# Kernel tuning notes

Hardware: AMD Instinct MI355X
Metric: run time of the kernel (lower is better)

The kernel has to match this reference:

```python
import jax, jax.numpy as jnp
import numpy as np

N = 8000   # nodes
E = 32000  # edges
B = 64     # graphs in batch
V = 5000   # vocab
D = 200    # embed dim; 20 tokens/node * 200 = 4000 = conv1 in_dim
T = 20


def setup_inputs() -> dict:
    key = jax.random.key(0)
    ks = jax.random.split(key, 12)
    return {
        "x": jax.random.randint(ks[0], (N, T), 0, V),
        "edge_index": jax.random.randint(ks[1], (2, E), 0, N),
        "batch": jnp.sort(jax.random.randint(ks[2], (N,), 0, B)),
        "emb": jax.random.normal(ks[3], (V, D), jnp.float32) * 0.02,
        "W1": jax.random.normal(ks[4], (4000, 6000), jnp.float32) * 0.01,
        "b1": jnp.zeros((6000,), jnp.float32),
        "W2": jax.random.normal(ks[5], (6000, 6000), jnp.float32) * 0.01,
        "b2": jnp.zeros((6000,), jnp.float32),
        "Wl1": jax.random.normal(ks[6], (6000, 3000), jnp.float32) * 0.01,
        "bl1": jnp.zeros((3000,), jnp.float32),
        "Wl2": jax.random.normal(ks[7], (3000, 4), jnp.float32) * 0.01,
        "bl2": jnp.zeros((4,), jnp.float32),
    }


def gcn_conv(h, W, b, src, dst, n):
    """PyG GCNConv: x' = D^-1/2 (A+I) D^-1/2 (x W) + b; src/dst include self-loops."""
    h = h @ W  # [n, out]
    deg = jax.ops.segment_sum(jnp.ones(dst.shape[0], h.dtype), dst, num_segments=n)
    dinv = jnp.where(deg > 0, jax.lax.rsqrt(deg), 0.0)
    norm = dinv[src] * dinv[dst]  # [E+n]
    agg = jax.ops.segment_sum(h[src] * norm[:, None], dst, num_segments=n)
    return agg + b


def reference(x, edge_index, batch, emb, W1, b1, W2, b2, Wl1, bl1, Wl2, bl2):
    n = x.shape[0]
    h = emb[x].reshape(n, -1)  # [N, 4000]
    loops = jnp.arange(n)
    src = jnp.concatenate([edge_index[0], loops])
    dst = jnp.concatenate([edge_index[1], loops])
    h = jax.nn.leaky_relu(gcn_conv(h, W1, b1, src, dst, n))  # dropout: identity in eval
    h = jax.nn.leaky_relu(gcn_conv(h, W2, b2, src, dst, n))
    g = jax.ops.segment_max(h, batch, num_segments=B)  # global_max_pool -> [B, 6000]
    g = jax.nn.leaky_relu(g @ Wl1 + bl1)
    return jax.nn.leaky_relu(g @ Wl2 + bl2)  # [B, 4]
```

## Files before the change

### kernel.cpp

```cpp
#include <hip/hip_runtime.h>
#include <hip/hip_bf16.h>

#define Nn 8000
#define Ee 32000
#define Bb 64
#define Dembed 200
#define Ttok 20
#define Mp 8192
#define K1 4096
#define K2 6144
#define L1p 3072
#define LCHUNK 256
#define NCH 24

#define GBM 256
#define GBN 256
#define GBK 64
#define ABUF (GBM * GBK)
#define BUFE (2 * ABUF)

#define LRELU(v) ((v) > 0.f ? (v) : 0.01f * (v))

typedef __attribute__((ext_vector_type(4))) float f32x4;
typedef __attribute__((ext_vector_type(8))) short s16x8;

#define GLL16(gp, lp) __builtin_amdgcn_global_load_lds( \
    (const __attribute__((address_space(1))) void*)(gp), \
    (__attribute__((address_space(3))) void*)(lp), 16, 0, 0)

__device__ __forceinline__ float b2f(short s) {
    union { unsigned u; float f; } c;
    c.u = ((unsigned)(unsigned short)s) << 16;
    return c.f;
}
__device__ __forceinline__ short f2b(float f) {
    __hip_bfloat16 h = __float2bfloat16(f);
    return __builtin_bit_cast(short, h);
}

__global__ __launch_bounds__(256)
void k_gather(const int* __restrict__ x, const float* __restrict__ emb,
              short* __restrict__ h0, int Wp)
{
    const int i = blockIdx.x;
    __shared__ int tok[Ttok];
    if (threadIdx.x < Ttok) tok[threadIdx.x] = x[i * Ttok + threadIdx.x];
    __syncthreads();
    for (int c = threadIdx.x; c < Wp; c += 256) {
        float v = 0.f;
        if (c < Ttok * Dembed) {
            int t = c / Dembed;
            int d = c - t * Dembed;
            v = emb[(long)tok[t] * Dembed + d];
        }
        h0[(long)i * Wp + c] = f2b(v);
    }
}

__global__ void k_deg(const int* __restrict__ dst, int* __restrict__ indeg) {
    int e = blockIdx.x * 256 + threadIdx.x;
    if (e < Ee) atomicAdd(&indeg[dst[e]], 1);
}

__global__ void k_dinv(const int* __restrict__ indeg, float* __restrict__ dinv) {
    int i = blockIdx.x * 256 + threadIdx.x;
    if (i < Nn) dinv[i] = rsqrtf((float)indeg[i] + 1.0f);
}

__global__ __launch_bounds__(1024)
void k_scan(const int* __restrict__ indeg, int* __restrict__ rowptr, int n)
{
    __shared__ int sums[1024];
    const int t = threadIdx.x;
    const int base = t * 8;
    int loc[8];
    int s = 0;
#pragma unroll
    for (int j = 0; j < 8; ++j) {
        int v = (base + j < n) ? indeg[base + j] : 0;
        loc[j] = s; s += v;
    }
    sums[t] = s;
    __syncthreads();
    for (int off = 1; off < 1024; off <<= 1) {
        int v = sums[t];
        int add = (t >= off) ? sums[t - off] : 0;
        __syncthreads();
        sums[t] = v + add;
        __syncthreads();
    }
    const int prev = (t == 0) ? 0 : sums[t - 1];
#pragma unroll
    for (int j = 0; j < 8; ++j)
        if (base + j < n) rowptr[base + j] = prev + loc[j];
    if (t == 1023) rowptr[n] = sums[1023];
}

__global__ void k_fill(const int* __restrict__ src, const int* __restrict__ dst,
                       const int* __restrict__ rowptr, int* __restrict__ fillc,
                       int* __restrict__ csr) {
    int e = blockIdx.x * 256 + threadIdx.x;
    if (e < Ee) {
        int d = dst[e];
        int pos = rowptr[d] + atomicAdd(&fillc[d], 1);
        csr[pos] = src[e];
    }
}

template<int NG>
__global__ __launch_bounds__(256)
void k_agg(const short* __restrict__ Hin, short* __restrict__ Hout,
           const float* __restrict__ dinv, const int* __restrict__ rowptr,
           const int* __restrict__ csr, int Wp)
{
    const int i = blockIdx.x;
    const int tid = threadIdx.x;
    const float di = dinv[i];
    const float wself = di * di;
    const long rowi = (long)i * Wp;
    float acc[NG * 8];
#pragma unroll
    for (int gI = 0; gI < NG; ++gI) {
        s16x8 v = *(const s16x8*)(Hin + rowi + gI * 2048 + tid * 8);
#pragma unroll
        for (int j = 0; j < 8; ++j) acc[gI * 8 + j] = wself * b2f(v[j]);
    }
    const int e0 = rowptr[i], e1 = rowptr[i + 1];
    for (int e = e0; e < e1; ++e) {
        const int s = csr[e];
        const float w = dinv[s] * di;
        const long rows = (long)s * Wp;
#pragma unroll
        for (int gI = 0; gI < NG; ++gI) {
            s16x8 v = *(const s16x8*)(Hin + rows + gI * 2048 + tid * 8);
#pragma unroll
            for (int j = 0; j < 8; ++j) acc[gI * 8 + j] += w * b2f(v[j]);
        }
    }
#pragma unroll
    for (int gI = 0; gI < NG; ++gI) {
        s16x8 o;
#pragma unroll
        for (int j = 0; j < 8; ++j) o[j] = f2b(acc[gI * 8 + j]);
        *(s16x8*)(Hout + rowi + gI * 2048 + tid * 8) = o;
    }
}

__global__ void k_transpose(const float* __restrict__ In, short* __restrict__ Out,
                            int K, int N, int Kp, int Np)
{
    __shared__ float tile[32][33];
    const int k0 = blockIdx.x * 32;
    const int n0 = blockIdx.y * 32;
    const int tx = threadIdx.x, ty = threadIdx.y;
#pragma unroll
    for (int yy = ty; yy < 32; yy += 8) {
        int k = k0 + yy, n = n0 + tx;
        tile[yy][tx] = (k < K && n < N) ? In[(long)k * N + n] : 0.f;
    }
    __syncthreads();
#pragma unroll
    for (int yy = ty; yy < 32; yy += 8) {
        int n = n0 + yy, k = k0 + tx;
        if (n < Np && k < Kp) Out[(long)n * Kp + k] = f2b(tile[tx][yy]);
    }
}

__global__ __launch_bounds__(512, 2)
void k_gemm8p(const short* __restrict__ A, const short* __restrict__ Bt,
              short* __restrict__ C, const float* __restrict__ bias,
              int K, int Np, int Nreal, int nbx)
{
    __shared__ short lds[2 * BUFE];

    const int tid  = threadIdx.x;
    const int lane = tid & 63;
    const int wid  = tid >> 6;
    const int wm   = wid >> 2;
    const int wn   = wid & 3;

    const int cpx = (int)gridDim.x >> 3;
    const int bid = (int)blockIdx.x;
    const int swz = (bid & 7) * cpx + (bid >> 3);
    const int bx = swz % nbx;
    const int by = swz / nbx;

    const int rq = tid >> 3;
    const int kq = ((tid & 7) << 3) ^ ((rq & 7) << 3);
    const short* Abase = A  + ((long)by * GBM + rq) * K + kq;
    const short* Bbase = Bt + ((long)bx * GBN + rq) * K + kq;

#define ST2(bb, t2, base, ldoff, c0_, c1_) do { \
    const short* g0_ = (base) + (long)((c0_) * 64) * K + (long)(t2) * GBK; \
    const short* g1_ = (base) + (long)((c1_) * 64) * K + (long)(t2) * GBK; \
    GLL16(g0_, lds + (bb) * BUFE + (ldoff) + (c0_) * 4096 + tid * 8); \
    GLL16(g1_, lds + (bb) * BUFE + (ldoff) + (c1_) * 4096 + tid * 8); \
  } while (0)

    const int fr  = lane & 15;
    const int kb8 = (lane >> 4) << 3;
    const int xm  = (fr & 7) << 3;
    const int ck0 = kb8 ^ xm;
    const int ck1 = (32 + kb8) ^ xm;
    const int aoff = (wm * 128 + fr) * 64;
    const int boff = ABUF + (wn * 64 + fr) * 64;

    f32x4 acc[8][4] = {};
    s16x8 av[4], bv[4];

    const int NT = K >> 6;

    ST2(0, 0, Bbase, ABUF, 0, 1);
    ST2(0, 0, Bbase, ABUF, 2, 3);
    ST2(0, 0, Abase, 0,    0, 2);
    ST2(0, 0, Abase, 0,    1, 3);
    ST2(1, 1, Bbase, ABUF, 0, 1);
    asm volatile("s_waitcnt vmcnt(4)" ::: "memory");
    __builtin_amdgcn_s_barrier();

    int buf = 0;
    for (int t = 0; t < NT; ++t) {
        const short* lb = lds + buf * BUFE;
        const int nb = buf ^ 1;
        const bool pf1 = (t + 1 < NT);
        const bool pf2 = (t + 2 < NT);

#pragma unroll
        for (int n = 0; n < 4; ++n) bv[n] = *(const s16x8*)(lb + boff + n * 1024 + ck0);
#pragma unroll
        for (int m = 0; m < 4; ++m) av[m] = *(const s16x8*)(lb + aoff + m * 1024 + ck0);
        if (pf1) ST2(nb, t + 1, Bbase, ABUF, 2, 3);
        __builtin_amdgcn_s_barrier();
        __builtin_amdgcn_s_setprio(1);
#pragma unroll
        for (int m = 0; m < 4; ++m)
#pragma unroll
            for (int n = 0; n < 4; ++n)
                acc[m][n] = __builtin_amdgcn_mfma_f32_16x16x32_bf16(av[m], bv[n], acc[m][n], 0, 0, 0);
        __builtin_amdgcn_s_setprio(0);
        if (pf1) asm volatile("s_waitcnt vmcnt(4)" ::: "memory");
        else     asm volatile("s_waitcnt vmcnt(0)" ::: "memory");
        __builtin_amdgcn_s_barrier();

#pragma unroll
        for (int m = 0; m < 4; ++m) av[m] = *(const s16x8*)(lb + aoff + (4 + m) * 1024 + ck0);
        if (pf1) ST2(nb, t + 1, Abase, 0, 0, 2);
        __builtin_amdgcn_s_barrier();
        __builtin_amdgcn_s_setprio(1);
#pragma unroll
        for (int m = 0; m < 4; ++m)
#pragma unroll
            for (int n = 0; n < 4; ++n)
                acc[4 + m][n] = __builtin_amdgcn_mfma_f32_16x16x32_bf16(av[m], bv[n], acc[4 + m][n], 0, 0, 0);
        __builtin_amdgcn_s_setprio(0);
        __builtin_amdgcn_s_barrier();

#pragma unroll
        for (int n = 0; n < 4; ++n) bv[n] = *(const s16x8*)(lb + boff + n * 1024 + ck1);
#pragma unroll
        for (int m = 0; m < 4; ++m) av[m] = *(const s16x8*)(lb + aoff + (4 + m) * 1024 + ck1);
        if (pf1) ST2(nb, t + 1, Abase, 0, 1, 3);
        __builtin_amdgcn_s_barrier();
        __builtin_amdgcn_s_setprio(1);
#pragma unroll
        for (int m = 0; m < 4; ++m)
#pragma unroll
            for (int n = 0; n < 4; ++n)
                acc[4 + m][n] = __builtin_amdgcn_mfma_f32_16x16x32_bf16(av[m], bv[n], acc[4 + m][n], 0, 0, 0);
        __builtin_amdgcn_s_setprio(0);
        __builtin_amdgcn_s_barrier();

#pragma unroll
        for (int m = 0; m < 4; ++m) av[m] = *(const s16x8*)(lb + aoff + m * 1024 + ck1);
        if (pf2) ST2(buf, t + 2, Bbase, ABUF, 0, 1);
        __builtin_amdgcn_s_barrier();
        __builtin_amdgcn_s_setprio(1);
#pragma unroll
        for (int m = 0; m < 4; ++m)
#pragma unroll
            for (int n = 0; n < 4; ++n)
                acc[m][n] = __builtin_amdgcn_mfma_f32_16x16x32_bf16(av[m], bv[n], acc[m][n], 0, 0, 0);
        __builtin_amdgcn_s_setprio(0);
        if (pf2)      asm volatile("s_waitcnt vmcnt(4)" ::: "memory");
        else if (pf1) asm volatile("s_waitcnt vmcnt(2)" ::: "memory");
        __builtin_amdgcn_s_barrier();

        buf = nb;
    }

    const int rr = (lane >> 4) << 2;
#pragma unroll
    for (int n = 0; n < 4; ++n) {
        const long col = (long)bx * GBN + wn * 64 + n * 16 + fr;
        const float bvv = (col < Nreal) ? bias[col] : 0.f;
#pragma unroll
        for (int m = 0; m < 8; ++m) {
#pragma unroll
            for (int j = 0; j < 4; ++j) {
                const long row = (long)by * GBM + wm * 128 + m * 16 + rr + j;
                float v = acc[m][n][j] + bvv;
                v = LRELU(v);
                C[row * Np + col] = f2b(v);
            }
        }
    }
#undef ST2
}

__global__ void k_bptr(const int* __restrict__ batch, int* __restrict__ bptr) {
    int i = blockIdx.x * 256 + threadIdx.x;
    if (i >= Nn) return;
    int b = batch[i];
    int pb = (i == 0) ? -1 : batch[i - 1];
    for (int bb = pb + 1; bb <= b; ++bb) bptr[bb] = i;
    if (i == Nn - 1)
        for (int bb = b + 1; bb <= Bb; ++bb) bptr[bb] = Nn;
}

__global__ __launch_bounds__(256)
void k_pool(const short* __restrict__ h2, const int* __restrict__ bptr,
            float* __restrict__ g, int Wp) {
    const int c8 = blockIdx.x * 256 + threadIdx.x;
    const int b = blockIdx.y;
    const short* base = h2 + (long)c8 * 8;
    float mx[8];
#pragma unroll
    for (int j = 0; j < 8; ++j) mx[j] = -INFINITY;
    const int i0 = bptr[b], i1 = bptr[b + 1];
    for (int i = i0; i < i1; ++i) {
        s16x8 v = *(const s16x8*)(base + (long)i * Wp);
#pragma unroll
        for (int j = 0; j < 8; ++j) mx[j] = fmaxf(mx[j], b2f(v[j]));
    }
#pragma unroll
    for (int j = 0; j < 8; ++j) g[(long)b * Wp + c8 * 8 + j] = mx[j];
}

__global__ __launch_bounds__(256)
void k_lin1_part(const float* __restrict__ g, const float* __restrict__ Wl1,
                 float* __restrict__ part) {
    __shared__ float gs[64][65];
    __shared__ float Ws[64][64];
    const int tid = threadIdx.x;
    const int jc = blockIdx.x * 64;
    const int k0 = blockIdx.y * LCHUNK;
    const int k1 = min(6000, k0 + LCHUNK);
    const int r = tid & 63;
    const int jb = (tid >> 6) * 16;
    float acc[16] = {};
    for (int kc = k0; kc < k1; kc += 64) {
#pragma unroll
        for (int p = 0; p < 16; ++p) {
            int el = p * 256 + tid;
            int rr = el >> 6, kk = el & 63;
            gs[rr][kk] = (kc + kk < k1) ? g[rr * K2 + kc + kk] : 0.f;
            Ws[rr][kk] = (kc + rr < k1 && jc + kk < 3000)
                         ? Wl1[(long)(kc + rr) * 3000 + jc + kk] : 0.f;
        }
        __syncthreads();
#pragma unroll
        for (int k = 0; k < 64; ++k) {
            float a = gs[r][k];
#pragma unroll
            for (int jj = 0; jj < 16; ++jj)
                acc[jj] += a * Ws[k][jb + jj];
        }
        __syncthreads();
    }
    float* prow = part + ((long)blockIdx.y * 64 + r) * L1p + jc + jb;
#pragma unroll
    for (int jj = 0; jj < 16; ++jj) prow[jj] = acc[jj];
}

__global__ __launch_bounds__(256)
void k_lin1_red(const float* __restrict__ part, const float* __restrict__ bl1,
                float* __restrict__ g1) {
    int idx = blockIdx.x * 256 + threadIdx.x;
    if (idx >= 64 * 3000) return;
    int r = idx / 3000;
    int c = idx - r * 3000;
    float s = bl1[c];
#pragma unroll
    for (int p = 0; p < NCH; ++p)
        s += part[((long)p * 64 + r) * L1p + c];
    g1[r * L1p + c] = LRELU(s);
}

__global__ __launch_bounds__(256)
void k_lin2(const float* __restrict__ g1, const float* __restrict__ Wl2,
            const float* __restrict__ bl2, float* __restrict__ out) {
    const int r = blockIdx.x;
    const int tid = threadIdx.x;
    float a0 = 0, a1 = 0, a2 = 0, a3 = 0;
    for (int k = tid; k < 3000; k += 256) {
        float gv = g1[r * L1p + k];
        const float* w = Wl2 + (long)k * 4;
        a0 += gv * w[0]; a1 += gv * w[1]; a2 += gv * w[2]; a3 += gv * w[3];
    }
    __shared__ float red[256][4];
    red[tid][0] = a0; red[tid][1] = a1; red[tid][2] = a2; red[tid][3] = a3;
    __syncthreads();
    for (int s = 128; s > 0; s >>= 1) {
        if (tid < s) {
            red[tid][0] += red[tid + s][0]; red[tid][1] += red[tid + s][1];
            red[tid][2] += red[tid + s][2]; red[tid][3] += red[tid + s][3];
        }
        __syncthreads();
    }
    if (tid < 4) {
        float v = red[0][tid] + bl2[tid];
        out[r * 4 + tid] = LRELU(v);
    }
}

extern "C" void kernel_launch(void* const* d_in, const int* in_sizes, int n_in,
                              void* d_out, int out_size, void* d_ws, size_t ws_size,
                              hipStream_t stream)
{
    const int*   x     = (const int*)d_in[0];
    const int*   ei    = (const int*)d_in[1];
    const int*   batch = (const int*)d_in[2];
    const float* emb   = (const float*)d_in[3];
    const float* W1    = (const float*)d_in[4];
    const float* b1    = (const float*)d_in[5];
    const float* W2    = (const float*)d_in[6];
    const float* b2    = (const float*)d_in[7];
    const float* Wl1   = (const float*)d_in[8];
    const float* bl1   = (const float*)d_in[9];
    const float* Wl2   = (const float*)d_in[10];
    const float* bl2   = (const float*)d_in[11];
    float* out = (float*)d_out;

    const int* esrc = ei;
    const int* edst = ei + Ee;

    const size_t MiB = 1ull << 20;
    char* W = (char*)d_ws;
    short* h0b  = (short*)(W + 0);
    short* Ah0b = (short*)(W + 64 * MiB);
    short* W2t  = (short*)(W + 96 * MiB);
    short* W1t  = (short*)(W + 128 * MiB);
    short* h1b  = (short*)(W + 176 * MiB);
    short* Ah1b = (short*)(W + 0);
    short* h2b  = h1b;
    float* part = (float*)(W + 0);
    char* S = W + 272 * MiB;
    int*   indeg  = (int*)(S);
    float* dinv   = (float*)(S + 32 * 1024);
    int*   rowptr = (int*)(S + 64 * 1024);
    int*   fillc  = (int*)(S + 96 * 1024);
    int*   csr    = (int*)(S + 128 * 1024);
    int*   bptr   = (int*)(S + 256 * 1024);
    float* g      = (float*)(S + 320 * 1024);
    float* g1     = (float*)(S + 320 * 1024 + 2 * MiB);

    hipMemsetAsync(indeg, 0, Nn * sizeof(int), stream);
    hipMemsetAsync(fillc, 0, Nn * sizeof(int), stream);

    k_gather<<<Nn, 256, 0, stream>>>(x, emb, h0b, K1);
    k_deg<<<(Ee + 255) / 256, 256, 0, stream>>>(edst, indeg);
    k_dinv<<<(Nn + 255) / 256, 256, 0, stream>>>(indeg, dinv);
    k_scan<<<1, 1024, 0, stream>>>(indeg, rowptr, Nn);
    k_fill<<<(Ee + 255) / 256, 256, 0, stream>>>(esrc, edst, rowptr, fillc, csr);

    const int nbx = K2 / GBN;
    const int nwg = nbx * (Mp / GBM);

    k_agg<2><<<Nn, 256, 0, stream>>>(h0b, Ah0b, dinv, rowptr, csr, K1);
    k_transpose<<<dim3(K1 / 32, K2 / 32), dim3(32, 8), 0, stream>>>(W1, W1t, 4000, 6000, K1, K2);
    k_gemm8p<<<nwg, 512, 0, stream>>>(Ah0b, W1t, h1b, b1, K1, K2, 6000, nbx);

    k_transpose<<<dim3(K2 / 32, K2 / 32), dim3(32, 8), 0, stream>>>(W2, W2t, 6000, 6000, K2, K2);
    k_agg<3><<<Nn, 256, 0, stream>>>(h1b, Ah1b, dinv, rowptr, csr, K2);
    k_gemm8p<<<nwg, 512, 0, stream>>>(Ah1b, W2t, h2b, b2, K2, K2, 6000, nbx);

    k_bptr<<<(Nn + 255) / 256, 256, 0, stream>>>(batch, bptr);
    k_pool<<<dim3(K2 / 2048, Bb), 256, 0, stream>>>(h2b, bptr, g, K2);
    k_lin1_part<<<dim3(L1p / 64, NCH), 256, 0, stream>>>(g, Wl1, part);
    k_lin1_red<<<(64 * 3000 + 255) / 256, 256, 0, stream>>>(part, bl1, g1);
    k_lin2<<<Bb, 256, 0, stream>>>(g1, Wl2, bl2, out);
}
```

Before: 1.393 ms.

## Restructure GEMM main loop to single-barrier double buffering; vectorize transpose; fuse dinv

The bf16 MFMA GEMM loop now uses a plain double buffer. Next-tile global-to-LDS loads are interleaved between four MFMA phases, with a single vmcnt(0) wait and one barrier per K-tile. This replaces the earlier staggered two-tile-ahead prefetch that needed many barriers per iteration, trading barrier overhead against less prefetch lead time. The weight transpose kernel now uses a flat 256-thread block and writes four packed bf16 values per thread. The dinv computation is folded into the scan kernel, removing one launch.

```diff
diff --git a/kernel.cpp b/kernel.cpp
--- a/kernel.cpp
+++ b/kernel.cpp
@@ -23,6 +23,7 @@
 
 typedef __attribute__((ext_vector_type(4))) float f32x4;
 typedef __attribute__((ext_vector_type(8))) short s16x8;
+typedef __attribute__((ext_vector_type(4))) short s16x4;
 
 #define GLL16(gp, lp) __builtin_amdgcn_global_load_lds( \
     (const __attribute__((address_space(1))) void*)(gp), \
@@ -62,13 +63,9 @@
     if (e < Ee) atomicAdd(&indeg[dst[e]], 1);
 }
 
-__global__ void k_dinv(const int* __restrict__ indeg, float* __restrict__ dinv) {
-    int i = blockIdx.x * 256 + threadIdx.x;
-    if (i < Nn) dinv[i] = rsqrtf((float)indeg[i] + 1.0f);
-}
-
 __global__ __launch_bounds__(1024)
-void k_scan(const int* __restrict__ indeg, int* __restrict__ rowptr, int n)
+void k_scan(const int* __restrict__ indeg, int* __restrict__ rowptr,
+            float* __restrict__ dinv, int n)
 {
     __shared__ int sums[1024];
     const int t = threadIdx.x;
@@ -92,7 +89,10 @@
     const int prev = (t == 0) ? 0 : sums[t - 1];
 #pragma unroll
     for (int j = 0; j < 8; ++j)
-        if (base + j < n) rowptr[base + j] = prev + loc[j];
+        if (base + j < n) {
+            rowptr[base + j] = prev + loc[j];
+            dinv[base + j] = rsqrtf((float)indeg[base + j] + 1.0f);
+        }
     if (t == 1023) rowptr[n] = sums[1023];
 }
 
@@ -146,24 +146,26 @@
     }
 }
 
-__global__ void k_transpose(const float* __restrict__ In, short* __restrict__ Out,
-                            int K, int N, int Kp, int Np)
+__global__ __launch_bounds__(256)
+void k_transpose(const float* __restrict__ In, short* __restrict__ Out,
+                 int K, int N, int Kp, int Np)
 {
     __shared__ float tile[32][33];
     const int k0 = blockIdx.x * 32;
     const int n0 = blockIdx.y * 32;
-    const int tx = threadIdx.x, ty = threadIdx.y;
-#pragma unroll
-    for (int yy = ty; yy < 32; yy += 8) {
-        int k = k0 + yy, n = n0 + tx;
-        tile[yy][tx] = (k < K && n < N) ? In[(long)k * N + n] : 0.f;
+    const int tid = threadIdx.x;
+    const int ln = tid & 31, lk = tid >> 5;
+#pragma unroll
+    for (int kk = lk; kk < 32; kk += 8) {
+        int k = k0 + kk, n = n0 + ln;
+        tile[kk][ln] = (k < K && n < N) ? In[(long)k * N + n] : 0.f;
     }
     __syncthreads();
-#pragma unroll
-    for (int yy = ty; yy < 32; yy += 8) {
-        int n = n0 + yy, k = k0 + tx;
-        if (n < Np && k < Kp) Out[(long)n * Kp + k] = f2b(tile[tx][yy]);
-    }
+    const int kq = tid & 7, nn = tid >> 3;
+    s16x4 o;
+#pragma unroll
+    for (int j = 0; j < 4; ++j) o[j] = f2b(tile[kq * 4 + j][nn]);
+    *(s16x4*)(&Out[(long)(n0 + nn) * Kp + k0 + kq * 4]) = o;
 }
 
 __global__ __launch_bounds__(512, 2)
@@ -206,7 +208,7 @@
     const int boff = ABUF + (wn * 64 + fr) * 64;
 
     f32x4 acc[8][4] = {};
-    s16x8 av[4], bv[4];
+    s16x8 av_a[4], av_b[4], bv1[4], bv3[4];
 
     const int NT = K >> 6;
 
@@ -214,77 +216,62 @@
     ST2(0, 0, Bbase, ABUF, 2, 3);
     ST2(0, 0, Abase, 0,    0, 2);
     ST2(0, 0, Abase, 0,    1, 3);
-    ST2(1, 1, Bbase, ABUF, 0, 1);
-    asm volatile("s_waitcnt vmcnt(4)" ::: "memory");
+    asm volatile("s_waitcnt vmcnt(0)" ::: "memory");
     __builtin_amdgcn_s_barrier();
 
     int buf = 0;
     for (int t = 0; t < NT; ++t) {
         const short* lb = lds + buf * BUFE;
         const int nb = buf ^ 1;
-        const bool pf1 = (t + 1 < NT);
-        const bool pf2 = (t + 2 < NT);
-
-#pragma unroll
-        for (int n = 0; n < 4; ++n) bv[n] = *(const s16x8*)(lb + boff + n * 1024 + ck0);
-#pragma unroll
-        for (int m = 0; m < 4; ++m) av[m] = *(const s16x8*)(lb + aoff + m * 1024 + ck0);
-        if (pf1) ST2(nb, t + 1, Bbase, ABUF, 2, 3);
+        const bool pf = (t + 1 < NT);
+
+#pragma unroll
+        for (int n = 0; n < 4; ++n) bv1[n] = *(const s16x8*)(lb + boff + n * 1024 + ck0);
+#pragma unroll
+        for (int m = 0; m < 4; ++m) av_a[m] = *(const s16x8*)(lb + aoff + m * 1024 + ck0);
+        if (pf) ST2(nb, t + 1, Bbase, ABUF, 0, 1);
+#pragma unroll
+        for (int m = 0; m < 4; ++m) av_b[m] = *(const s16x8*)(lb + aoff + (4 + m) * 1024 + ck0);
+        __builtin_amdgcn_s_setprio(1);
+#pragma unroll
+        for (int m = 0; m < 4; ++m)
+#pragma unroll
+            for (int n = 0; n < 4; ++n)
+                acc[m][n] = __builtin_amdgcn_mfma_f32_16x16x32_bf16(av_a[m], bv1[n], acc[m][n], 0, 0, 0);
+        __builtin_amdgcn_s_setprio(0);
+        if (pf) ST2(nb, t + 1, Bbase, ABUF, 2, 3);
+#pragma unroll
+        for (int n = 0; n < 4; ++n) bv3[n] = *(const s16x8*)(lb + boff + n * 1024 + ck1);
+#pragma unroll
+        for (int m = 0; m < 4; ++m) av_a[m] = *(const s16x8*)(lb + aoff + (4 + m) * 1024 + ck1);
+        __builtin_amdgcn_s_setprio(1);
+#pragma unroll
+        for (int m = 0; m < 4; ++m)
+#pragma unroll
+            for (int n = 0; n < 4; ++n)
+                acc[4 + m][n] = __builtin_amdgcn_mfma_f32_16x16x32_bf16(av_b[m], bv1[n], acc[4 + m][n], 0, 0, 0);
+        __builtin_amdgcn_s_setprio(0);
+        if (pf) ST2(nb, t + 1, Abase, 0, 0, 2);
+#pragma unroll
+        for (int m = 0; m < 4; ++m) av_b[m] = *(const s16x8*)(lb + aoff + m * 1024 + ck1);
+        __builtin_amdgcn_s_setprio(1);
+#pragma unroll
+        for (int m = 0; m < 4; ++m)
+#pragma unroll
+            for (int n = 0; n < 4; ++n)
+                acc[4 + m][n] = __builtin_amdgcn_mfma_f32_16x16x32_bf16(av_a[m], bv3[n], acc[4 + m][n], 0, 0, 0);
+        __builtin_amdgcn_s_setprio(0);
+        if (pf) ST2(nb, t + 1, Abase, 0, 1, 3);
+        __builtin_amdgcn_s_setprio(1);
+#pragma unroll
+        for (int m = 0; m < 4; ++m)
+#pragma unroll
+            for (int n = 0; n < 4; ++n)
+                acc[m][n] = __builtin_amdgcn_mfma_f32_16x16x32_bf16(av_b[m], bv3[n], acc[m][n], 0, 0, 0);
+        __builtin_amdgcn_s_setprio(0);
+
+        asm volatile("s_waitcnt vmcnt(0)" ::: "memory");
         __builtin_amdgcn_s_barrier();
-        __builtin_amdgcn_s_setprio(1);
-#pragma unroll
-        for (int m = 0; m < 4; ++m)
-#pragma unroll
-            for (int n = 0; n < 4; ++n)
-                acc[m][n] = __builtin_amdgcn_mfma_f32_16x16x32_bf16(av[m], bv[n], acc[m][n], 0, 0, 0);
-        __builtin_amdgcn_s_setprio(0);
-        if (pf1) asm volatile("s_waitcnt vmcnt(4)" ::: "memory");
-        else     asm volatile("s_waitcnt vmcnt(0)" ::: "memory");
-        __builtin_amdgcn_s_barrier();
-
-#pragma unroll
-        for (int m = 0; m < 4; ++m) av[m] = *(const s16x8*)(lb + aoff + (4 + m) * 1024 + ck0);
-        if (pf1) ST2(nb, t + 1, Abase, 0, 0, 2);
-        __builtin_amdgcn_s_barrier();
-        __builtin_amdgcn_s_setprio(1);
-#pragma unroll
-        for (int m = 0; m < 4; ++m)
-#pragma unroll
-            for (int n = 0; n < 4; ++n)
-                acc[4 + m][n] = __builtin_amdgcn_mfma_f32_16x16x32_bf16(av[m], bv[n], acc[4 + m][n], 0, 0, 0);
-        __builtin_amdgcn_s_setprio(0);
-        __builtin_amdgcn_s_barrier();
-
-#pragma unroll
-        for (int n = 0; n < 4; ++n) bv[n] = *(const s16x8*)(lb + boff + n * 1024 + ck1);
-#pragma unroll
-        for (int m = 0; m < 4; ++m) av[m] = *(const s16x8*)(lb + aoff + (4 + m) * 1024 + ck1);
-        if (pf1) ST2(nb, t + 1, Abase, 0, 1, 3);
-        __builtin_amdgcn_s_barrier();
-        __builtin_amdgcn_s_setprio(1);
-#pragma unroll
-        for (int m = 0; m < 4; ++m)
-#pragma unroll
-            for (int n = 0; n < 4; ++n)
-                acc[4 + m][n] = __builtin_amdgcn_mfma_f32_16x16x32_bf16(av[m], bv[n], acc[4 + m][n], 0, 0, 0);
-        __builtin_amdgcn_s_setprio(0);
-        __builtin_amdgcn_s_barrier();
-
-#pragma unroll
-        for (int m = 0; m < 4; ++m) av[m] = *(const s16x8*)(lb + aoff + m * 1024 + ck1);
-        if (pf2) ST2(buf, t + 2, Bbase, ABUF, 0, 1);
-        __builtin_amdgcn_s_barrier();
-        __builtin_amdgcn_s_setprio(1);
-#pragma unroll
-        for (int m = 0; m < 4; ++m)
-#pragma unroll
-            for (int n = 0; n < 4; ++n)
-                acc[m][n] = __builtin_amdgcn_mfma_f32_16x16x32_bf16(av[m], bv[n], acc[m][n], 0, 0, 0);
-        __builtin_amdgcn_s_setprio(0);
-        if (pf2)      asm volatile("s_waitcnt vmcnt(4)" ::: "memory");
-        else if (pf1) asm volatile("s_waitcnt vmcnt(2)" ::: "memory");
-        __builtin_amdgcn_s_barrier();
-
         buf = nb;
     }
 
@@ -459,18 +446,17 @@
 
     k_gather<<<Nn, 256, 0, stream>>>(x, emb, h0b, K1);
     k_deg<<<(Ee + 255) / 256, 256, 0, stream>>>(edst, indeg);
-    k_dinv<<<(Nn + 255) / 256, 256, 0, stream>>>(indeg, dinv);
-    k_scan<<<1, 1024, 0, stream>>>(indeg, rowptr, Nn);
+    k_scan<<<1, 1024, 0, stream>>>(indeg, rowptr, dinv, Nn);
     k_fill<<<(Ee + 255) / 256, 256, 0, stream>>>(esrc, edst, rowptr, fillc, csr);
 
     const int nbx = K2 / GBN;
     const int nwg = nbx * (Mp / GBM);
 
     k_agg<2><<<Nn, 256, 0, stream>>>(h0b, Ah0b, dinv, rowptr, csr, K1);
-    k_transpose<<<dim3(K1 / 32, K2 / 32), dim3(32, 8), 0, stream>>>(W1, W1t, 4000, 6000, K1, K2);
+    k_transpose<<<dim3(K1 / 32, K2 / 32), 256, 0, stream>>>(W1, W1t, 4000, 6000, K1, K2);
     k_gemm8p<<<nwg, 512, 0, stream>>>(Ah0b, W1t, h1b, b1, K1, K2, 6000, nbx);
 
-    k_transpose<<<dim3(K2 / 32, K2 / 32), dim3(32, 8), 0, stream>>>(W2, W2t, 6000, 6000, K2, K2);
+    k_transpose<<<dim3(K2 / 32, K2 / 32), 256, 0, stream>>>(W2, W2t, 6000, 6000, K2, K2);
     k_agg<3><<<Nn, 256, 0, stream>>>(h1b, Ah1b, dinv, rowptr, csr, K2);
     k_gemm8p<<<nwg, 512, 0, stream>>>(Ah1b, W2t, h2b, b2, K2, K2, 6000, nbx);
 
```

Measured after the change: 1.402 ms. About the same (+0.6%).
